# Kernel optimization log

Measured on AMD Instinct MI355X. Metric: run time of the kernel, lower is better.

## Reference

```python
import jax, jax.numpy as jnp
import numpy as np

N_HEADS = 32
N_KV_HEADS = 8
HEAD_DIM = 128
N_QUERY = N_HEADS // N_KV_HEADS  # 4
ROPE_BASE = 10000.0


def _rope_tables(seq_len, head_dim):
    # inv freqs over pairs of channels (Llama-style interleaved complex rotation)
    inv_freq = 1.0 / (ROPE_BASE ** (jnp.arange(0, head_dim, 2, dtype=jnp.float32) / head_dim))
    t = jnp.arange(seq_len, dtype=jnp.float32)
    ang = t[:, None] * inv_freq[None, :]           # [s, d/2]
    return jnp.cos(ang)[None, :, None, :], jnp.sin(ang)[None, :, None, :]  # [1,s,1,d/2]


def _apply_rope(x, cos, sin):
    # x: [b, s, h, d]; consecutive channel pairs are (real, imag)
    xr = x[..., 0::2]
    xi = x[..., 1::2]
    out_r = xr * cos - xi * sin
    out_i = xr * sin + xi * cos
    return jnp.stack([out_r, out_i], axis=-1).reshape(x.shape)


def setup_inputs() -> dict:
    key = jax.random.key(0)
    kx, kq, kk, kv, ko = jax.random.split(key, 5)
    dim = 4096
    kv_dim = N_KV_HEADS * HEAD_DIM
    scale = 0.02
    return {
        "x": jax.random.normal(kx, (2, 2048, dim), dtype=jnp.float32),
        "wq": jax.random.normal(kq, (dim, dim), dtype=jnp.float32) * scale,
        "wk": jax.random.normal(kk, (dim, kv_dim), dtype=jnp.float32) * scale,
        "wv": jax.random.normal(kv, (dim, kv_dim), dtype=jnp.float32) * scale,
        "wo": jax.random.normal(ko, (dim, dim), dtype=jnp.float32) * scale,
    }


def reference(x, wq, wk, wv, wo):
    b, s, _ = x.shape
    xq = (x @ wq).reshape(b, s, N_HEADS, HEAD_DIM)
    xk = (x @ wk).reshape(b, s, N_KV_HEADS, HEAD_DIM)
    xv = (x @ wv).reshape(b, s, N_KV_HEADS, HEAD_DIM)

    cos, sin = _rope_tables(s, HEAD_DIM)
    xq = _apply_rope(xq, cos, sin)
    xk = _apply_rope(xk, cos, sin)

    # GQA without materializing the KV expand: group query heads per kv head.
    qh = xq.reshape(b, s, N_KV_HEADS, N_QUERY, HEAD_DIM)
    scores = jnp.einsum('bsgnd,btgd->bgnst', qh, xk) / jnp.sqrt(
        jnp.asarray(HEAD_DIM, dtype=xq.dtype))  # [b,g,n,s,t]

    # causal mask: -inf above diagonal
    causal = jnp.arange(s)[:, None] >= jnp.arange(s)[None, :]
    scores = jnp.where(causal[None, None, None, :, :], scores, -jnp.inf)

    att = jax.nn.softmax(scores.astype(jnp.float32), axis=-1).astype(xq.dtype)
    out = jnp.einsum('bgnst,btgd->bsgnd', att, xv).reshape(b, s, N_HEADS * HEAD_DIM)
    return out @ wo
```

## Files before the change

kernel.cpp:

```cpp
#include <hip/hip_runtime.h>
#include <hip/hip_bf16.h>

typedef __attribute__((ext_vector_type(8))) short short8;
typedef __attribute__((ext_vector_type(4))) float f32x4;
typedef __attribute__((ext_vector_type(16))) float f32x16;

#define GLD16(gp, lp) __builtin_amdgcn_global_load_lds( \
    (const __attribute__((address_space(1))) unsigned int*)(gp), \
    (__attribute__((address_space(3))) unsigned int*)(lp), 16, 0, 0)

static __device__ __forceinline__ float bf2f(unsigned short u) {
    union { unsigned int i; float f; } v; v.i = ((unsigned int)u) << 16; return v.f;
}
static __device__ __forceinline__ short f2bf(float f) {
    union { float f; unsigned int i; } v; v.f = f;
    unsigned int r = v.i + 0x7FFFu + ((v.i >> 16) & 1u);
    return (short)(r >> 16);
}
static __device__ __forceinline__ unsigned int pack2bf(float lo, float hi) {
    return ((unsigned int)(unsigned short)f2bf(hi) << 16) | (unsigned int)(unsigned short)f2bf(lo);
}
static __device__ __forceinline__ unsigned int cvtpk(float lo, float hi) {
    unsigned int w;
    asm("v_cvt_pk_bf16_f32 %0, %1, %2" : "=v"(w) : "v"(lo), "v"(hi));
    return w;
}

__global__ void cast_f32_bf16(const float* __restrict__ src, short* __restrict__ dst, int n) {
    int i = (blockIdx.x * 256 + threadIdx.x) * 4;
    if (i >= n) return;
    float4 v = *(const float4*)(src + i);
    short4 o;
    o.x = f2bf(v.x); o.y = f2bf(v.y); o.z = f2bf(v.z); o.w = f2bf(v.w);
    *(short4*)(dst + i) = o;
}

__global__ void transpose_cast(const float* __restrict__ src, short* __restrict__ dst,
                               int N, int dstStride) {
    __shared__ float tile[32][33];
    int k0 = blockIdx.x * 32, n0 = blockIdx.y * 32;
    int t = threadIdx.x, c = t & 31, r = t >> 5;
#pragma unroll
    for (int p = 0; p < 4; ++p)
        tile[r + p * 8][c] = src[(size_t)(k0 + r + p * 8) * N + n0 + c];
    __syncthreads();
#pragma unroll
    for (int p = 0; p < 4; ++p)
        dst[(size_t)(n0 + r + p * 8) * dstStride + k0 + c] = f2bf(tile[c][r + p * 8]);
}

__global__ void transpose_v(const short* __restrict__ qkv, short* __restrict__ vt) {
    __shared__ short tile[32][33];
    int s0 = blockIdx.x * 32, d0 = blockIdx.y * 32;
    int bh = blockIdx.z;
    int b = bh >> 3, h = bh & 7;
    const short* src = qkv + (size_t)b * 2048 * 6144 + 5120 + h * 128;
    short* dst = vt + (size_t)bh * 128 * 2048;
    int t = threadIdx.x, c = t & 31, r = t >> 5;
#pragma unroll
    for (int p = 0; p < 4; ++p)
        tile[r + p * 8][c] = src[(size_t)(s0 + r + p * 8) * 6144 + d0 + c];
    __syncthreads();
#pragma unroll
    for (int p = 0; p < 4; ++p)
        dst[(size_t)(d0 + r + p * 8) * 2048 + s0 + c] = tile[c][r + p * 8];
}

__global__ void rope_tables(float* __restrict__ cs) {
    int i = blockIdx.x * 256 + threadIdx.x;
    int s = i >> 6, d2 = i & 63;
    float inv = expf(-9.210340371976184f * (float)(2 * d2) * (1.0f / 128.0f));
    float ang = (float)s * inv;
    float sn, c;
    sincosf(ang, &sn, &c);
    cs[(size_t)i * 2] = c;
    cs[(size_t)i * 2 + 1] = sn;
}

template<int NH>
__global__ void rope_apply(const short* __restrict__ qkv, const float* __restrict__ cs,
                           short* __restrict__ dst, int colOff, float scale) {
    int i = blockIdx.x * 256 + threadIdx.x;
    int d2 = i & 63;
    int t2 = i >> 6;
    int h = t2 % NH;
    int bs = t2 / NH;
    int s = bs & 2047;
    int b = bs >> 11;
    unsigned int pr = *(const unsigned int*)(qkv + (size_t)bs * 6144 + colOff + h * 128 + 2 * d2);
    float xr = bf2f((unsigned short)(pr & 0xFFFFu));
    float xi = bf2f((unsigned short)(pr >> 16));
    const float* cp = cs + ((size_t)s * 64 + d2) * 2;
    float c = cp[0], sn = cp[1];
    float outr = (xr * c - xi * sn) * scale;
    float outi = (xr * sn + xi * c) * scale;
    *(unsigned int*)(dst + ((size_t)(b * NH + h) * 2048 + s) * 128 + 2 * d2) = pack2bf(outr, outi);
}

template<bool BF16OUT>
__global__ __launch_bounds__(512, 1) void gemm256(const short* __restrict__ A,
                                                  const short* __restrict__ Bt,
                                                  void* __restrict__ Cv,
                                                  int Mtiles, int N, int K) {
    extern __shared__ __align__(16) short lds[];
    short* As = lds;
    short* Bs = lds + 32768;
    const int tid = threadIdx.x;
    const int lane = tid & 63;
    const int wid = tid >> 6;
    const int lr = lane & 15;
    const int lq = lane >> 4;
    const int wr = wid >> 2;
    const int wc = wid & 3;

    const int nwg = gridDim.x;
    const int id = blockIdx.x;
    const int sid = (id & 7) * (nwg >> 3) + (id >> 3);
    const int m0 = (sid % Mtiles) * 256;
    const int n0 = (sid / Mtiles) * 256;

    const short* aBase = A + (size_t)m0 * K;
    const short* bBase = Bt + (size_t)n0 * K;
    const int NT = K >> 5;

    auto stageA = [&](int t) {
        const int buf = t & 3;
#pragma unroll
        for (int j = 0; j < 2; ++j) {
            int cl = j * 512 + tid;
            int lrw = cl >> 3;
            int cs = (cl & 7) ^ (lrw & 7);
            int trow = lrw + ((cs & 4) << 5);
            int kc = (cs & 3) * 8;
            GLD16(aBase + (size_t)trow * K + t * 32 + kc, As + buf * 8192 + cl * 8);
        }
    };
    auto stageB = [&](int t) {
        const int buf = t & 3;
#pragma unroll
        for (int j = 0; j < 2; ++j) {
            int cl = j * 512 + tid;
            int lrw = cl >> 3;
            int cs = (cl & 7) ^ (lrw & 7);
            int trow = lrw + ((cs & 4) << 5);
            int kc = (cs & 3) * 8;
            GLD16(bBase + (size_t)trow * K + t * 32 + kc, Bs + buf * 8192 + cl * 8);
        }
    };

    f32x4 acc[8][4];
#pragma unroll
    for (int mi = 0; mi < 8; ++mi)
#pragma unroll
        for (int ni = 0; ni < 4; ++ni) acc[mi][ni] = f32x4{0.f, 0.f, 0.f, 0.f};

    stageA(0); stageB(0); stageA(1); stageB(1); stageA(2); stageB(2);
    asm volatile("s_waitcnt vmcnt(8)" ::: "memory");
    __builtin_amdgcn_sched_barrier(0);
    __builtin_amdgcn_s_barrier();
    __builtin_amdgcn_sched_barrier(0);

    for (int t = 0; t < NT; ++t) {
        const int buf = t & 3;
        short8 af[8], bfr[4];

#pragma unroll
        for (int mi = 0; mi < 4; ++mi) {
            int lrw = mi * 16 + lr;
            int chunk = ((wr << 2) | lq) ^ (lrw & 7);
            af[mi] = *(const short8*)(As + buf * 8192 + lrw * 64 + chunk * 8);
        }
#pragma unroll
        for (int ni = 0; ni < 4; ++ni) {
            int tc = wc * 64 + ni * 16 + lr;
            int lrw = tc & 127;
            int chunk = (((tc >> 7) << 2) | lq) ^ (lrw & 7);
            bfr[ni] = *(const short8*)(Bs + buf * 8192 + lrw * 64 + chunk * 8);
        }
        if (t + 3 < NT) stageA(t + 3);
        __builtin_amdgcn_sched_barrier(0);
        __builtin_amdgcn_s_barrier();
        asm volatile("s_waitcnt lgkmcnt(0)" ::: "memory");
        __builtin_amdgcn_sched_barrier(0);
        __builtin_amdgcn_s_setprio(1);
#pragma unroll
        for (int mi = 0; mi < 4; ++mi)
#pragma unroll
            for (int ni = 0; ni < 4; ++ni)
                acc[mi][ni] = __builtin_amdgcn_mfma_f32_16x16x32_bf16(af[mi], bfr[ni], acc[mi][ni], 0, 0, 0);
        __builtin_amdgcn_s_setprio(0);
        __builtin_amdgcn_sched_barrier(0);
        __builtin_amdgcn_s_barrier();
        __builtin_amdgcn_sched_barrier(0);

#pragma unroll
        for (int mi = 4; mi < 8; ++mi) {
            int lrw = mi * 16 + lr;
            int chunk = ((wr << 2) | lq) ^ (lrw & 7);
            af[mi] = *(const short8*)(As + buf * 8192 + lrw * 64 + chunk * 8);
        }
        if (t + 3 < NT) stageB(t + 3);
        __builtin_amdgcn_sched_barrier(0);
        __builtin_amdgcn_s_barrier();
        asm volatile("s_waitcnt lgkmcnt(0)" ::: "memory");
        __builtin_amdgcn_sched_barrier(0);
        __builtin_amdgcn_s_setprio(1);
#pragma unroll
        for (int mi = 4; mi < 8; ++mi)
#pragma unroll
            for (int ni = 0; ni < 4; ++ni)
                acc[mi][ni] = __builtin_amdgcn_mfma_f32_16x16x32_bf16(af[mi], bfr[ni], acc[mi][ni], 0, 0, 0);
        __builtin_amdgcn_s_setprio(0);
        __builtin_amdgcn_sched_barrier(0);

        if (t + 3 < NT)       { asm volatile("s_waitcnt vmcnt(8)" ::: "memory"); }
        else if (t + 3 == NT) { asm volatile("s_waitcnt vmcnt(4)" ::: "memory"); }
        else if (t + 2 == NT) { asm volatile("s_waitcnt vmcnt(0)" ::: "memory"); }
        __builtin_amdgcn_sched_barrier(0);
        if (t + 1 < NT) {
            __builtin_amdgcn_s_barrier();
            __builtin_amdgcn_sched_barrier(0);
        }
    }

#pragma unroll
    for (int mi = 0; mi < 8; ++mi)
#pragma unroll
        for (int ni = 0; ni < 4; ++ni)
#pragma unroll
            for (int r = 0; r < 4; ++r) {
                int row = m0 + wr * 128 + mi * 16 + lq * 4 + r;
                int col = n0 + wc * 64 + ni * 16 + lr;
                float v = acc[mi][ni][r];
                if constexpr (BF16OUT) ((short*)Cv)[(size_t)row * N + col] = f2bf(v);
                else                   ((float*)Cv)[(size_t)row * N + col] = v;
            }
}

__global__ __launch_bounds__(256, 2) void attn_kernel(const short* __restrict__ Qr,
                                                      const short* __restrict__ Kr,
                                                      const short* __restrict__ Vt,
                                                      short* __restrict__ Out) {
    __shared__ short Ks[64 * 128];
    __shared__ short Vs[128 * 64];
    const int qb = 15 - blockIdx.x;
    const int bh = blockIdx.y;
    const int b = bh >> 5;
    const int qh = bh & 31;
    const int kvh = qh >> 2;
    const int tid = threadIdx.x;
    const int lane = tid & 63;
    const int w = tid >> 6;
    const int l31 = lane & 31;
    const int hi = lane >> 5;
    const int qg0 = qb * 128 + w * 32;

    const short* qbase = Qr + ((size_t)bh * 2048 + qg0 + l31) * 128 + hi * 8;
    short8 qf[8];
#pragma unroll
    for (int ks = 0; ks < 8; ++ks)
        qf[ks] = *(const short8*)(qbase + ks * 16);

    const short* kbase = Kr + (size_t)(b * 8 + kvh) * 2048 * 128;
    const short* vbase = Vt + (size_t)(b * 8 + kvh) * 128 * 2048;

    float m_run = -INFINITY, l_run = 0.0f;
    f32x16 oacc[4];
#pragma unroll
    for (int dt = 0; dt < 4; ++dt) oacc[dt] = f32x16{0,0,0,0,0,0,0,0,0,0,0,0,0,0,0,0};

    const int nkb = 2 * qb + 2;
    for (int kb = 0; kb < nkb; ++kb) {
        const int s0 = kb * 64;
#pragma unroll
        for (int j = 0; j < 4; ++j) {
            int c = j * 256 + tid;
            int krow = c >> 4;
            int kcol = ((c & 15) ^ (krow & 7)) * 8;
            GLD16(kbase + (size_t)(s0 + krow) * 128 + kcol, Ks + (size_t)c * 8);
            int vrow = c >> 3;
            int vcol = ((c & 7) ^ (vrow & 7)) * 8;
            GLD16(vbase + (size_t)vrow * 2048 + s0 + vcol, Vs + (size_t)c * 8);
        }
        __syncthreads();

        if (s0 <= qg0 + 31) {
            f32x16 st0 = f32x16{0,0,0,0,0,0,0,0,0,0,0,0,0,0,0,0};
            f32x16 st1 = f32x16{0,0,0,0,0,0,0,0,0,0,0,0,0,0,0,0};
            __builtin_amdgcn_s_setprio(1);
#pragma unroll
            for (int ks = 0; ks < 8; ++ks) {
                int row0 = l31;
                int ch0 = ((2 * ks + hi) ^ (row0 & 7)) * 8;
                short8 kf0 = *(const short8*)(Ks + row0 * 128 + ch0);
                st0 = __builtin_amdgcn_mfma_f32_32x32x16_bf16(kf0, qf[ks], st0, 0, 0, 0);
                int row1 = 32 + l31;
                int ch1 = ((2 * ks + hi) ^ (row1 & 7)) * 8;
                short8 kf1 = *(const short8*)(Ks + row1 * 128 + ch1);
                st1 = __builtin_amdgcn_mfma_f32_32x32x16_bf16(kf1, qf[ks], st1, 0, 0, 0);
            }
            __builtin_amdgcn_s_setprio(0);

            const int q = qg0 + l31;
            if (s0 + 63 > qg0) {
#pragma unroll
                for (int i = 0; i < 16; ++i) {
                    int kvr = (i & 3) + 8 * (i >> 2) + 4 * hi;
                    if (s0 + kvr > q)      st0[i] = -INFINITY;
                    if (s0 + 32 + kvr > q) st1[i] = -INFINITY;
                }
            }

            float mx = -INFINITY;
#pragma unroll
            for (int i = 0; i < 16; ++i) mx = fmaxf(mx, fmaxf(st0[i], st1[i]));
            mx = fmaxf(mx, __shfl_xor(mx, 32, 64));

            const bool defer = __all(mx - m_run <= 8.0f);
            float mN, alpha;
            if (defer) { mN = m_run; alpha = 1.0f; }
            else       { mN = fmaxf(m_run, mx); alpha = __expf(m_run - mN); }

            float p0[16], p1[16];
            float rsum = 0.0f;
#pragma unroll
            for (int i = 0; i < 16; ++i) {
                p0[i] = __expf(st0[i] - mN);
                p1[i] = __expf(st1[i] - mN);
                rsum += p0[i] + p1[i];
            }
            rsum += __shfl_xor(rsum, 32, 64);
            l_run = l_run * alpha + rsum;
            m_run = mN;
            if (!defer) {
#pragma unroll
                for (int dt = 0; dt < 4; ++dt)
#pragma unroll
                    for (int i = 0; i < 16; ++i) oacc[dt][i] *= alpha;
            }

            short8 pfr[4];
#pragma unroll
            for (int kvs = 0; kvs < 4; ++kvs) {
                const float* pp = (kvs < 2) ? p0 : p1;
                const int h8 = (kvs & 1) * 8;
                unsigned int x0 = cvtpk(pp[h8 + 0], pp[h8 + 1]);
                unsigned int x1 = cvtpk(pp[h8 + 2], pp[h8 + 3]);
                unsigned int y0 = cvtpk(pp[h8 + 4], pp[h8 + 5]);
                unsigned int y1 = cvtpk(pp[h8 + 6], pp[h8 + 7]);
                asm("v_permlane32_swap_b32 %0, %1" : "+v"(x0), "+v"(y0));
                asm("v_permlane32_swap_b32 %0, %1" : "+v"(x1), "+v"(y1));
                union { unsigned int u[4]; short8 s; } uu;
                uu.u[0] = x0; uu.u[1] = x1; uu.u[2] = y0; uu.u[3] = y1;
                pfr[kvs] = uu.s;
            }

            __builtin_amdgcn_s_setprio(1);
#pragma unroll
            for (int dt = 0; dt < 4; ++dt) {
                int row = dt * 32 + l31;
#pragma unroll
                for (int kvs = 0; kvs < 4; ++kvs) {
                    int ch = ((2 * kvs + hi) ^ (row & 7)) * 8;
                    short8 vf = *(const short8*)(Vs + row * 64 + ch);
                    oacc[dt] = __builtin_amdgcn_mfma_f32_32x32x16_bf16(vf, pfr[kvs], oacc[dt], 0, 0, 0);
                }
            }
            __builtin_amdgcn_s_setprio(0);
        }
        __syncthreads();
    }

    const float inv = 1.0f / l_run;
    const size_t row = (size_t)b * 2048 + qg0 + l31;
    short* obase = Out + row * 4096 + qh * 128;
#pragma unroll
    for (int dt = 0; dt < 4; ++dt) {
#pragma unroll
        for (int g = 0; g < 4; ++g) {
            short4 o4;
            o4.x = f2bf(oacc[dt][g * 4 + 0] * inv);
            o4.y = f2bf(oacc[dt][g * 4 + 1] * inv);
            o4.z = f2bf(oacc[dt][g * 4 + 2] * inv);
            o4.w = f2bf(oacc[dt][g * 4 + 3] * inv);
            *(short4*)(obase + dt * 32 + g * 8 + hi * 4) = o4;
        }
    }
}


extern "C" void kernel_launch(void* const* d_in, const int* in_sizes, int n_in,
                              void* d_out, int out_size, void* d_ws, size_t ws_size,
                              hipStream_t stream) {
    const float* x  = (const float*)d_in[0];
    const float* wq = (const float*)d_in[1];
    const float* wk = (const float*)d_in[2];
    const float* wv = (const float*)d_in[3];
    const float* wo = (const float*)d_in[4];
    float* out = (float*)d_out;
    char* ws = (char*)d_ws;

    short* wt_qkv = (short*)(ws + 0);
    short* xb     = (short*)(ws + 50331648);
    short* qkv    = (short*)(ws + 83886080);
    short* wt_o   = (short*)(ws + 83886080);
    short* qr     = (short*)(ws + 134217728);
    short* kr     = (short*)(ws + 167772160);
    short* vt     = (short*)(ws + 176160768);
    float* tab    = (float*)(ws + 184549376);

    cast_f32_bf16<<<16384, 256, 0, stream>>>(x, xb, 16777216);
    transpose_cast<<<dim3(128, 128), 256, 0, stream>>>(wq, wt_qkv, 4096, 4096);
    transpose_cast<<<dim3(128, 32),  256, 0, stream>>>(wk, wt_qkv + (size_t)4096 * 4096, 1024, 4096);
    transpose_cast<<<dim3(128, 32),  256, 0, stream>>>(wv, wt_qkv + (size_t)5120 * 4096, 1024, 4096);
    rope_tables<<<512, 256, 0, stream>>>(tab);
    gemm256<true><<<384, 512, 131072, stream>>>(xb, wt_qkv, (void*)qkv, 16, 6144, 4096);
    rope_apply<32><<<32768, 256, 0, stream>>>(qkv, tab, qr, 0, 0.08838834764831845f);
    rope_apply<8><<<8192, 256, 0, stream>>>(qkv, tab, kr, 4096, 1.0f);
    transpose_v<<<dim3(64, 4, 16), 256, 0, stream>>>(qkv, vt);
    transpose_cast<<<dim3(128, 128), 256, 0, stream>>>(wo, wt_o, 4096, 4096);
    attn_kernel<<<dim3(16, 64), 256, 0, stream>>>(qr, kr, vt, xb);
    gemm256<false><<<256, 512, 131072, stream>>>(xb, wt_o, (void*)out, 16, 4096, 4096);
}
```

Before: 623.8 us.

## Restructure GEMM main loop to 64-wide K tiles with quadrant ping-pong staging

The 256x256 GEMM's K loop moves from 32-wide k-steps with four buffers to 64-wide k-steps with two buffers. Each buffer is split into A and B halves. Each iteration now runs four MFMA phases over quadrant pairs (A-low/B-low, A-low/B-high, A-high/B-high, A-high/B-low) and issues next-tile loads for one half-tile per phase. The aim is to halve per-iteration barrier and loop overhead while keeping loads overlapped with MFMAs. In exchange it adds two extra barriers per iteration and shortens prefetch depth, and it relies on subtle vmcnt accounting that could cause races.

```diff
diff --git a/kernel.cpp b/kernel.cpp
--- a/kernel.cpp
+++ b/kernel.cpp
@@ -103,8 +103,6 @@
                                                   void* __restrict__ Cv,
                                                   int Mtiles, int N, int K) {
     extern __shared__ __align__(16) short lds[];
-    short* As = lds;
-    short* Bs = lds + 32768;
     const int tid = threadIdx.x;
     const int lane = tid & 63;
     const int wid = tid >> 6;
@@ -121,30 +119,28 @@
 
     const short* aBase = A + (size_t)m0 * K;
     const short* bBase = Bt + (size_t)n0 * K;
-    const int NT = K >> 5;
-
-    auto stageA = [&](int t) {
-        const int buf = t & 3;
+    const int NT = K >> 6;
+
+    auto stageA = [&](int t, int X) {
+        const int base = ((t & 1) * 2 + X) * 8192;
 #pragma unroll
         for (int j = 0; j < 2; ++j) {
             int cl = j * 512 + tid;
             int lrw = cl >> 3;
             int cs = (cl & 7) ^ (lrw & 7);
-            int trow = lrw + ((cs & 4) << 5);
-            int kc = (cs & 3) * 8;
-            GLD16(aBase + (size_t)trow * K + t * 32 + kc, As + buf * 8192 + cl * 8);
+            int row = (lrw & 63) + ((lrw >> 6) << 7) + (X << 6);
+            GLD16(aBase + (size_t)row * K + t * 64 + cs * 8, lds + base + cl * 8);
         }
     };
-    auto stageB = [&](int t) {
-        const int buf = t & 3;
+    auto stageB = [&](int t, int X) {
+        const int base = 32768 + ((t & 1) * 2 + X) * 8192;
 #pragma unroll
         for (int j = 0; j < 2; ++j) {
             int cl = j * 512 + tid;
             int lrw = cl >> 3;
             int cs = (cl & 7) ^ (lrw & 7);
-            int trow = lrw + ((cs & 4) << 5);
-            int kc = (cs & 3) * 8;
-            GLD16(bBase + (size_t)trow * K + t * 32 + kc, Bs + buf * 8192 + cl * 8);
+            int row = (lrw & 31) + ((lrw >> 5) << 6) + (X << 5);
+            GLD16(bBase + (size_t)row * K + t * 64 + cs * 8, lds + base + cl * 8);
         }
     };
 
@@ -154,68 +150,117 @@
 #pragma unroll
         for (int ni = 0; ni < 4; ++ni) acc[mi][ni] = f32x4{0.f, 0.f, 0.f, 0.f};
 
-    stageA(0); stageB(0); stageA(1); stageB(1); stageA(2); stageB(2);
-    asm volatile("s_waitcnt vmcnt(8)" ::: "memory");
+    stageA(0, 0); stageB(0, 0); stageB(0, 1); stageA(0, 1); stageA(1, 0); stageB(1, 1);
+    asm volatile("s_waitcnt vmcnt(4)" ::: "memory");
     __builtin_amdgcn_sched_barrier(0);
     __builtin_amdgcn_s_barrier();
     __builtin_amdgcn_sched_barrier(0);
 
+    const int a_lrw0 = wr * 64 + lr;
+    const int b_lrw0 = wc * 32 + lr;
+
     for (int t = 0; t < NT; ++t) {
-        const int buf = t & 3;
-        short8 af[8], bfr[4];
+        const short* Abuf = lds + (t & 1) * 2 * 8192;
+        const short* Bbuf = lds + 32768 + (t & 1) * 2 * 8192;
+        short8 af[4][2], bl[2][2], bh[2][2];
 
 #pragma unroll
         for (int mi = 0; mi < 4; ++mi) {
-            int lrw = mi * 16 + lr;
-            int chunk = ((wr << 2) | lq) ^ (lrw & 7);
-            af[mi] = *(const short8*)(As + buf * 8192 + lrw * 64 + chunk * 8);
-        }
-#pragma unroll
-        for (int ni = 0; ni < 4; ++ni) {
-            int tc = wc * 64 + ni * 16 + lr;
-            int lrw = tc & 127;
-            int chunk = (((tc >> 7) << 2) | lq) ^ (lrw & 7);
-            bfr[ni] = *(const short8*)(Bs + buf * 8192 + lrw * 64 + chunk * 8);
-        }
-        if (t + 3 < NT) stageA(t + 3);
+            int lrw = a_lrw0 + mi * 16;
+#pragma unroll
+            for (int ks = 0; ks < 2; ++ks)
+                af[mi][ks] = *(const short8*)(Abuf + lrw * 64 + (((ks * 4 + lq) ^ (lrw & 7)) * 8));
+        }
+#pragma unroll
+        for (int ni = 0; ni < 2; ++ni) {
+            int lrw = b_lrw0 + ni * 16;
+#pragma unroll
+            for (int ks = 0; ks < 2; ++ks)
+                bl[ni][ks] = *(const short8*)(Bbuf + lrw * 64 + (((ks * 4 + lq) ^ (lrw & 7)) * 8));
+        }
+        if (t + 1 < NT) stageA(t + 1, 1);
         __builtin_amdgcn_sched_barrier(0);
         __builtin_amdgcn_s_barrier();
         asm volatile("s_waitcnt lgkmcnt(0)" ::: "memory");
         __builtin_amdgcn_sched_barrier(0);
         __builtin_amdgcn_s_setprio(1);
 #pragma unroll
-        for (int mi = 0; mi < 4; ++mi)
-#pragma unroll
-            for (int ni = 0; ni < 4; ++ni)
-                acc[mi][ni] = __builtin_amdgcn_mfma_f32_16x16x32_bf16(af[mi], bfr[ni], acc[mi][ni], 0, 0, 0);
+        for (int ks = 0; ks < 2; ++ks)
+#pragma unroll
+            for (int mi = 0; mi < 4; ++mi)
+#pragma unroll
+                for (int ni = 0; ni < 2; ++ni)
+                    acc[mi][ni] = __builtin_amdgcn_mfma_f32_16x16x32_bf16(af[mi][ks], bl[ni][ks], acc[mi][ni], 0, 0, 0);
         __builtin_amdgcn_s_setprio(0);
         __builtin_amdgcn_sched_barrier(0);
         __builtin_amdgcn_s_barrier();
         __builtin_amdgcn_sched_barrier(0);
 
 #pragma unroll
-        for (int mi = 4; mi < 8; ++mi) {
-            int lrw = mi * 16 + lr;
-            int chunk = ((wr << 2) | lq) ^ (lrw & 7);
-            af[mi] = *(const short8*)(As + buf * 8192 + lrw * 64 + chunk * 8);
-        }
-        if (t + 3 < NT) stageB(t + 3);
+        for (int ni = 0; ni < 2; ++ni) {
+            int lrw = b_lrw0 + ni * 16;
+#pragma unroll
+            for (int ks = 0; ks < 2; ++ks)
+                bh[ni][ks] = *(const short8*)(Bbuf + 8192 + lrw * 64 + (((ks * 4 + lq) ^ (lrw & 7)) * 8));
+        }
+        if (t + 1 < NT) stageB(t + 1, 0);
         __builtin_amdgcn_sched_barrier(0);
         __builtin_amdgcn_s_barrier();
         asm volatile("s_waitcnt lgkmcnt(0)" ::: "memory");
         __builtin_amdgcn_sched_barrier(0);
         __builtin_amdgcn_s_setprio(1);
 #pragma unroll
-        for (int mi = 4; mi < 8; ++mi)
-#pragma unroll
-            for (int ni = 0; ni < 4; ++ni)
-                acc[mi][ni] = __builtin_amdgcn_mfma_f32_16x16x32_bf16(af[mi], bfr[ni], acc[mi][ni], 0, 0, 0);
+        for (int ks = 0; ks < 2; ++ks)
+#pragma unroll
+            for (int mi = 0; mi < 4; ++mi)
+#pragma unroll
+                for (int ni = 0; ni < 2; ++ni)
+                    acc[mi][ni + 2] = __builtin_amdgcn_mfma_f32_16x16x32_bf16(af[mi][ks], bh[ni][ks], acc[mi][ni + 2], 0, 0, 0);
         __builtin_amdgcn_s_setprio(0);
         __builtin_amdgcn_sched_barrier(0);
-
-        if (t + 3 < NT)       { asm volatile("s_waitcnt vmcnt(8)" ::: "memory"); }
-        else if (t + 3 == NT) { asm volatile("s_waitcnt vmcnt(4)" ::: "memory"); }
-        else if (t + 2 == NT) { asm volatile("s_waitcnt vmcnt(0)" ::: "memory"); }
+        __builtin_amdgcn_s_barrier();
+        __builtin_amdgcn_sched_barrier(0);
+
+#pragma unroll
+        for (int mi = 0; mi < 4; ++mi) {
+            int lrw = a_lrw0 + mi * 16;
+#pragma unroll
+            for (int ks = 0; ks < 2; ++ks)
+                af[mi][ks] = *(const short8*)(Abuf + 8192 + lrw * 64 + (((ks * 4 + lq) ^ (lrw & 7)) * 8));
+        }
+        if (t + 2 < NT) stageA(t + 2, 0);
+        __builtin_amdgcn_sched_barrier(0);
+        __builtin_amdgcn_s_barrier();
+        asm volatile("s_waitcnt lgkmcnt(0)" ::: "memory");
+        __builtin_amdgcn_sched_barrier(0);
+        __builtin_amdgcn_s_setprio(1);
+#pragma unroll
+        for (int ks = 0; ks < 2; ++ks)
+#pragma unroll
+            for (int mi = 0; mi < 4; ++mi)
+#pragma unroll
+                for (int ni = 0; ni < 2; ++ni)
+                    acc[mi + 4][ni + 2] = __builtin_amdgcn_mfma_f32_16x16x32_bf16(af[mi][ks], bh[ni][ks], acc[mi + 4][ni + 2], 0, 0, 0);
+        __builtin_amdgcn_s_setprio(0);
+        __builtin_amdgcn_sched_barrier(0);
+        __builtin_amdgcn_s_barrier();
+        __builtin_amdgcn_sched_barrier(0);
+
+        if (t + 2 < NT) stageB(t + 2, 1);
+        __builtin_amdgcn_sched_barrier(0);
+        __builtin_amdgcn_s_barrier();
+        __builtin_amdgcn_sched_barrier(0);
+        __builtin_amdgcn_s_setprio(1);
+#pragma unroll
+        for (int ks = 0; ks < 2; ++ks)
+#pragma unroll
+            for (int mi = 0; mi < 4; ++mi)
+#pragma unroll
+                for (int ni = 0; ni < 2; ++ni)
+                    acc[mi + 4][ni] = __builtin_amdgcn_mfma_f32_16x16x32_bf16(af[mi][ks], bl[ni][ks], acc[mi + 4][ni], 0, 0, 0);
+        __builtin_amdgcn_s_setprio(0);
+        __builtin_amdgcn_sched_barrier(0);
+        asm volatile("s_waitcnt vmcnt(4)" ::: "memory");
         __builtin_amdgcn_sched_barrier(0);
         if (t + 1 < NT) {
             __builtin_amdgcn_s_barrier();
```

Result: faster. 603.0 us (-3.3%).
